# Performance work log

Measured on AMD Instinct MI355X. Metric: run time of the kernel, lower is better.

Reference implementation:

```python
import jax, jax.numpy as jnp
import numpy as np

B, N, H = 4, 512, 64
EDGE_IN = 2 * H + 4

def silu(x):
    return x * jax.nn.sigmoid(x)

def setup_inputs() -> dict:
    key = jax.random.key(0)
    ks = jax.random.split(key, 16)
    def w(k, fan_in, fan_out):
        return (jax.random.normal(k, (fan_in, fan_out), jnp.float32) / np.sqrt(fan_in)).astype(jnp.float32)
    return {
        "h":   jax.random.normal(ks[0], (B, N, H), jnp.float32),
        "pos": jax.random.normal(ks[1], (B, N, 2), jnp.float32),
        "vel": jax.random.normal(ks[2], (B, N, 2), jnp.float32),
        # edge_mlp: Linear(2H+4,H) SiLU Linear(H,H) SiLU
        "ew1": w(ks[3], EDGE_IN, H), "eb1": jnp.zeros((H,), jnp.float32),
        "ew2": w(ks[4], H, H),       "eb2": jnp.zeros((H,), jnp.float32),
        # force_mlp: Linear(H,H) SiLU Linear(H,1)
        "fw1": w(ks[5], H, H),       "fb1": jnp.zeros((H,), jnp.float32),
        "fw2": w(ks[6], H, 1),       "fb2": jnp.zeros((1,), jnp.float32),
        # node_mlp: Linear(2H,H) SiLU Linear(H,H)
        "nw1": w(ks[7], 2 * H, H),   "nb1": jnp.zeros((H,), jnp.float32),
        "nw2": w(ks[8], H, H),       "nb2": jnp.zeros((H,), jnp.float32),
    }

def reference(h, pos, vel, ew1, eb1, ew2, eb2, fw1, fb1, fw2, fb2, nw1, nb1, nw2, nb2):
    b, n, hd = h.shape
    # rel_pos[b,i,j] = pos[b,j] - pos[b,i]  (torch: pos.unsqueeze(1) - pos.unsqueeze(2))
    rel_pos = pos[:, None, :, :] - pos[:, :, None, :]                # (B,N,N,2)
    dist_sq = jnp.sum(rel_pos ** 2, axis=-1, keepdims=True)         # (B,N,N,1)
    dist = jnp.sqrt(dist_sq + 1e-8)
    normal = rel_pos / dist                                          # (B,N,N,2)
    speed_sq = jnp.sum(vel ** 2, axis=-1, keepdims=True)             # (B,N,1)
    rel_vel = vel[:, None, :, :] - vel[:, :, None, :]                # (B,N,N,2)
    approach = jnp.sum(rel_vel * normal, axis=-1, keepdims=True)     # (B,N,N,1)
    h_i = jnp.broadcast_to(h[:, :, None, :], (b, n, n, hd))
    h_j = jnp.broadcast_to(h[:, None, :, :], (b, n, n, hd))
    sp_i = jnp.broadcast_to(speed_sq[:, :, None, :], (b, n, n, 1))
    sp_j = jnp.broadcast_to(speed_sq[:, None, :, :], (b, n, n, 1))
    edge_feat = jnp.concatenate([h_i, h_j, dist_sq, sp_i, sp_j, approach], axis=-1)  # (B,N,N,2H+4)
    m_ij = silu(silu(edge_feat @ ew1 + eb1) @ ew2 + eb2)             # (B,N,N,H)
    force_weight = silu(m_ij @ fw1 + fb1) @ fw2 + fb2                # (B,N,N,1)
    force_ij = force_weight * normal                                 # (B,N,N,2)
    mask = (1.0 - jnp.eye(n, dtype=h.dtype))[None, :, :, None]       # zero self-edges
    force = jnp.sum(force_ij * mask, axis=2)                         # (B,N,2)
    m_agg = jnp.sum(m_ij * mask, axis=2)                             # (B,N,H)
    h_new = silu(jnp.concatenate([h, m_agg], axis=-1) @ nw1 + nb1) @ nw2 + nb2  # (B,N,H)
    return (h_new, force)
```

## Files before the change

### kernel.cpp

```cpp
#include <hip/hip_runtime.h>
#include <hip/hip_bf16.h>
#include <stdint.h>

#define NB 4
#define NN 512
#define NH 64

typedef __attribute__((ext_vector_type(4))) float f32x4;
typedef __attribute__((ext_vector_type(8))) short short8;

__device__ __forceinline__ unsigned short bf16b(float f){
  union { float f; uint32_t u; } c; c.f = f;
  uint32_t u = c.u;
  u += 0x7fffu + ((u >> 16) & 1u);
  return (unsigned short)(u >> 16);
}
__device__ __forceinline__ uint32_t pk2(float lo, float hi){
  return (uint32_t)bf16b(lo) | ((uint32_t)bf16b(hi) << 16);
}
__device__ __forceinline__ float silu(float x){
  float e = __expf(-x);
  return x * __builtin_amdgcn_rcpf(1.0f + e);
}

__global__ void k_precompute_ac(const float* __restrict__ h,
                                const float* __restrict__ vel,
                                const float* __restrict__ ew1,
                                const float* __restrict__ eb1,
                                float* __restrict__ wa, float* __restrict__ wc){
  const int row = blockIdx.x;
  const int t = threadIdx.x;
  const float* hr = h + row * NH;
  const float vx = vel[row*2], vy = vel[row*2+1];
  const float sp = vx*vx + vy*vy;
  float aa = eb1[t] + sp * ew1[129*NH + t];
  float cc =          sp * ew1[130*NH + t];
  #pragma unroll 8
  for (int k = 0; k < NH; ++k){
    float hk = hr[k];
    aa += hk * ew1[k*NH + t];
    cc += hk * ew1[(NH + k)*NH + t];
  }
  wa[row*NH + t] = aa;
  wc[row*NH + t] = cc;
}

__global__ void k_frag_weights(const float* __restrict__ ew2,
                               const float* __restrict__ fw1,
                               unsigned short* __restrict__ wef,
                               unsigned short* __restrict__ wff){
  const int idx = blockIdx.x * blockDim.x + threadIdx.x;
  const int mat = idx >> 12;
  const int r = idx & 4095;
  const int e2 = r & 7;
  const int lane = (r >> 3) & 63;
  const int mtkk = r >> 9;
  const int kk = mtkk >> 2, mt = mtkk & 3;
  const int krow = kk*32 + (lane >> 4)*8 + e2;
  const int col  = mt*16 + (lane & 15);
  const float* W = mat ? fw1 : ew2;
  unsigned short v = bf16b(W[krow*NH + col]);
  if (mat) wff[r] = v; else wef[r] = v;
}

__launch_bounds__(256)
__global__ void k_edges(const float* __restrict__ pos,
                        const float* __restrict__ vel,
                        const float* __restrict__ wa,
                        const float* __restrict__ wc,
                        const float* __restrict__ ew1,
                        const float* __restrict__ eb2,
                        const float* __restrict__ fb1,
                        const float* __restrict__ fw2,
                        const float* __restrict__ fb2,
                        const unsigned short* __restrict__ wef,
                        const unsigned short* __restrict__ wff,
                        float* __restrict__ wmagg,
                        float* __restrict__ outF){
  const int row = blockIdx.x;
  const int b = row >> 9;
  const int i = row & (NN - 1);
  const int tid = threadIdx.x;
  const int l = tid & 63;
  const int w = tid >> 6;
  const int e = l & 15;
  const int g = l >> 4;
  const int bN = b * NN;

  const float pix = pos[row*2], piy = pos[row*2+1];
  const float vix = vel[row*2], viy = vel[row*2+1];
  const float fb2s = fb2[0];

  const float* arow = wa + row * NH;
  const f32x4 af0a = *(const f32x4*)(arow + 8*g);
  const f32x4 af0b = *(const f32x4*)(arow + 8*g + 4);
  const f32x4 af1a = *(const f32x4*)(arow + 32 + 8*g);
  const f32x4 af1b = *(const f32x4*)(arow + 32 + 8*g + 4);
  const float* wD = ew1 + 128*NH;
  const f32x4 d0a = *(const f32x4*)(wD + 8*g);
  const f32x4 d0b = *(const f32x4*)(wD + 8*g + 4);
  const f32x4 d1a = *(const f32x4*)(wD + 32 + 8*g);
  const f32x4 d1b = *(const f32x4*)(wD + 32 + 8*g + 4);
  const float* wP = ew1 + 131*NH;
  const f32x4 p0a = *(const f32x4*)(wP + 8*g);
  const f32x4 p0b = *(const f32x4*)(wP + 8*g + 4);
  const f32x4 p1a = *(const f32x4*)(wP + 32 + 8*g);
  const f32x4 p1b = *(const f32x4*)(wP + 32 + 8*g + 4);

  short8 aw[2][4], fw[2][4];
  #pragma unroll
  for (int kk = 0; kk < 2; ++kk){
    #pragma unroll
    for (int mt = 0; mt < 4; ++mt){
      aw[kk][mt] = *(const short8*)(wef + ((kk*4 + mt)*64 + l)*8);
      fw[kk][mt] = *(const short8*)(wff + ((kk*4 + mt)*64 + l)*8);
    }
  }

  f32x4 magg[4];
  #pragma unroll
  for (int mt = 0; mt < 4; ++mt) magg[mt] = (f32x4){0.f,0.f,0.f,0.f};
  float fx = 0.f, fy = 0.f;

  for (int it = 0; it < 8; ++it){
    const int jbase = (w + 4*it) * 16;
    const int j = jbase + e;
    const float2 pj = *(const float2*)(pos + (bN + j)*2);
    const float2 vj = *(const float2*)(vel + (bN + j)*2);
    const float rx = pj.x - pix, ry = pj.y - piy;
    const float ds = rx*rx + ry*ry;
    const float inv = __builtin_amdgcn_rsqf(ds + 1e-8f);
    const float nx = rx*inv, ny = ry*inv;
    const float ap = (vj.x - vix)*nx + (vj.y - viy)*ny;
    const float maskv = (j != i) ? 1.0f : 0.0f;

    const float* crow = wc + (bN + j)*NH;
    const f32x4 c0a = *(const f32x4*)(crow + 8*g);
    const f32x4 c0b = *(const f32x4*)(crow + 8*g + 4);
    const f32x4 c1a = *(const f32x4*)(crow + 32 + 8*g);
    const f32x4 c1b = *(const f32x4*)(crow + 32 + 8*g + 4);

    short8 bx[2];
    {
      union { uint32_t u[4]; short8 s; } cv;
      float s0 = silu(af0a.x + c0a.x + ds*d0a.x + ap*p0a.x);
      float s1 = silu(af0a.y + c0a.y + ds*d0a.y + ap*p0a.y);
      float s2 = silu(af0a.z + c0a.z + ds*d0a.z + ap*p0a.z);
      float s3 = silu(af0a.w + c0a.w + ds*d0a.w + ap*p0a.w);
      cv.u[0] = pk2(s0, s1); cv.u[1] = pk2(s2, s3);
      float s4 = silu(af0b.x + c0b.x + ds*d0b.x + ap*p0b.x);
      float s5 = silu(af0b.y + c0b.y + ds*d0b.y + ap*p0b.y);
      float s6 = silu(af0b.z + c0b.z + ds*d0b.z + ap*p0b.z);
      float s7 = silu(af0b.w + c0b.w + ds*d0b.w + ap*p0b.w);
      cv.u[2] = pk2(s4, s5); cv.u[3] = pk2(s6, s7);
      bx[0] = cv.s;
    }
    {
      union { uint32_t u[4]; short8 s; } cv;
      float s0 = silu(af1a.x + c1a.x + ds*d1a.x + ap*p1a.x);
      float s1 = silu(af1a.y + c1a.y + ds*d1a.y + ap*p1a.y);
      float s2 = silu(af1a.z + c1a.z + ds*d1a.z + ap*p1a.z);
      float s3 = silu(af1a.w + c1a.w + ds*d1a.w + ap*p1a.w);
      cv.u[0] = pk2(s0, s1); cv.u[1] = pk2(s2, s3);
      float s4 = silu(af1b.x + c1b.x + ds*d1b.x + ap*p1b.x);
      float s5 = silu(af1b.y + c1b.y + ds*d1b.y + ap*p1b.y);
      float s6 = silu(af1b.z + c1b.z + ds*d1b.z + ap*p1b.z);
      float s7 = silu(af1b.w + c1b.w + ds*d1b.w + ap*p1b.w);
      cv.u[2] = pk2(s4, s5); cv.u[3] = pk2(s6, s7);
      bx[1] = cv.s;
    }

    f32x4 accm[4];
    #pragma unroll
    for (int mt = 0; mt < 4; ++mt){
      accm[mt] = *(const f32x4*)(eb2 + mt*16 + 4*g);
      accm[mt] = __builtin_amdgcn_mfma_f32_16x16x32_bf16(aw[0][mt], bx[0], accm[mt], 0, 0, 0);
      accm[mt] = __builtin_amdgcn_mfma_f32_16x16x32_bf16(aw[1][mt], bx[1], accm[mt], 0, 0, 0);
    }

    uint32_t pkm[4][2];
    #pragma unroll
    for (int mt = 0; mt < 4; ++mt){
      float m0 = silu(accm[mt].x);
      float m1 = silu(accm[mt].y);
      float m2 = silu(accm[mt].z);
      float m3 = silu(accm[mt].w);
      magg[mt].x += maskv * m0;
      magg[mt].y += maskv * m1;
      magg[mt].z += maskv * m2;
      magg[mt].w += maskv * m3;
      pkm[mt][0] = pk2(m0, m1);
      pkm[mt][1] = pk2(m2, m3);
    }

    short8 bm[2];
    #pragma unroll
    for (int kk = 0; kk < 2; ++kk){
      union { uint32_t u[4]; short8 s; } cv;
      #pragma unroll
      for (int s = 0; s < 4; ++s){
        const int srcLane = (((s >> 1) + 2*(g & 1)) << 4) + e;
        uint32_t v0 = (uint32_t)__shfl((int)pkm[2*kk    ][s & 1], srcLane);
        uint32_t v1 = (uint32_t)__shfl((int)pkm[2*kk + 1][s & 1], srcLane);
        cv.u[s] = (g < 2) ? v0 : v1;
      }
      bm[kk] = cv.s;
    }

    float p = 0.f;
    #pragma unroll
    for (int mt = 0; mt < 4; ++mt){
      f32x4 acc2 = *(const f32x4*)(fb1 + mt*16 + 4*g);
      acc2 = __builtin_amdgcn_mfma_f32_16x16x32_bf16(fw[0][mt], bm[0], acc2, 0, 0, 0);
      acc2 = __builtin_amdgcn_mfma_f32_16x16x32_bf16(fw[1][mt], bm[1], acc2, 0, 0, 0);
      const f32x4 f2v = *(const f32x4*)(fw2 + mt*16 + 4*g);
      p += silu(acc2.x) * f2v.x;
      p += silu(acc2.y) * f2v.y;
      p += silu(acc2.z) * f2v.z;
      p += silu(acc2.w) * f2v.w;
    }
    p += __shfl_xor(p, 16);
    p += __shfl_xor(p, 32);
    const float fwt = p + fb2s;
    fx += maskv * fwt * nx;
    fy += maskv * fwt * ny;
  }

  __shared__ float smagg[4][64];
  __shared__ float sforce[4][2];

  #pragma unroll
  for (int mt = 0; mt < 4; ++mt){
    #pragma unroll
    for (int r = 0; r < 4; ++r){
      float v = magg[mt][r];
      v += __shfl_xor(v, 1);
      v += __shfl_xor(v, 2);
      v += __shfl_xor(v, 4);
      v += __shfl_xor(v, 8);
      if (e == 0) smagg[w][mt*16 + 4*g + r] = v;
    }
  }
  fx += __shfl_xor(fx, 1); fx += __shfl_xor(fx, 2); fx += __shfl_xor(fx, 4); fx += __shfl_xor(fx, 8);
  fy += __shfl_xor(fy, 1); fy += __shfl_xor(fy, 2); fy += __shfl_xor(fy, 4); fy += __shfl_xor(fy, 8);
  if (l == 0){ sforce[w][0] = fx; sforce[w][1] = fy; }
  __syncthreads();

  if (tid < 64)
    wmagg[row*NH + tid] = smagg[0][tid] + smagg[1][tid] + smagg[2][tid] + smagg[3][tid];
  if (tid == 0){
    outF[row*2]     = sforce[0][0] + sforce[1][0] + sforce[2][0] + sforce[3][0];
    outF[row*2 + 1] = sforce[0][1] + sforce[1][1] + sforce[2][1] + sforce[3][1];
  }
}

__global__ void k_node(const float* __restrict__ h,
                       const float* __restrict__ wmagg,
                       const float* __restrict__ nw1,
                       const float* __restrict__ nb1,
                       const float* __restrict__ nw2,
                       const float* __restrict__ nb2,
                       float* __restrict__ outH){
  const int row = blockIdx.x;
  const int t = threadIdx.x;
  __shared__ float t1[64];
  const float* hr = h + row * NH;
  const float* mr = wmagg + row * NH;
  float acc = nb1[t];
  #pragma unroll 8
  for (int k = 0; k < NH; ++k) acc += hr[k] * nw1[k*NH + t];
  #pragma unroll 8
  for (int k = 0; k < NH; ++k) acc += mr[k] * nw1[(NH + k)*NH + t];
  t1[t] = silu(acc);
  __syncthreads();
  float o = nb2[t];
  #pragma unroll 8
  for (int k = 0; k < NH; ++k) o += t1[k] * nw2[k*NH + t];
  outH[row*NH + t] = o;
}

extern "C" void kernel_launch(void* const* d_in, const int* in_sizes, int n_in,
                              void* d_out, int out_size, void* d_ws, size_t ws_size,
                              hipStream_t stream){
  const float* h   = (const float*)d_in[0];
  const float* pos = (const float*)d_in[1];
  const float* vel = (const float*)d_in[2];
  const float* ew1 = (const float*)d_in[3];
  const float* eb1 = (const float*)d_in[4];
  const float* ew2 = (const float*)d_in[5];
  const float* eb2 = (const float*)d_in[6];
  const float* fw1 = (const float*)d_in[7];
  const float* fb1 = (const float*)d_in[8];
  const float* fw2 = (const float*)d_in[9];
  const float* fb2 = (const float*)d_in[10];
  const float* nw1 = (const float*)d_in[11];
  const float* nb1 = (const float*)d_in[12];
  const float* nw2 = (const float*)d_in[13];
  const float* nb2 = (const float*)d_in[14];
  float* out = (float*)d_out;

  float* wa    = (float*)d_ws;
  float* wc    = wa + NB*NN*NH;
  float* wmagg = wc + NB*NN*NH;
  unsigned short* wef = (unsigned short*)(wmagg + NB*NN*NH);
  unsigned short* wff = wef + 4096;

  k_precompute_ac<<<dim3(NB*NN), dim3(64), 0, stream>>>(h, vel, ew1, eb1, wa, wc);
  k_frag_weights<<<dim3(32), dim3(256), 0, stream>>>(ew2, fw1, wef, wff);
  k_edges<<<dim3(NB*NN), dim3(256), 0, stream>>>(pos, vel, wa, wc, ew1, eb2, fb1, fw2, fb2,
                                                 wef, wff, wmagg, out + NB*NN*NH);
  k_node<<<dim3(NB*NN), dim3(64), 0, stream>>>(h, wmagg, nw1, nb1, nw2, nb2, out);
}
```

Measured before the change: 188.5 us.

## Merge precompute kernels, prefetch edge loads, pack node rows, use bf16 intrinsic

Merges the two precompute kernels into one launch, with extra blocks converting the weight fragments. The edge loop now software-prefetches the next iteration's pos, vel and wc loads into registers and is kept rolled, and k_edges gets a min-blocks launch bound. The node kernel handles four rows per 256-thread block instead of one row per 64-thread block, and bf16 packing uses the HIP float2-to-bfloat162 intrinsic. These aim to cut launch overhead and hide load latency, at the cost of higher register pressure in the edge kernel.

```diff
diff --git a/kernel.cpp b/kernel.cpp
--- a/kernel.cpp
+++ b/kernel.cpp
@@ -16,20 +16,43 @@
   return (unsigned short)(u >> 16);
 }
 __device__ __forceinline__ uint32_t pk2(float lo, float hi){
-  return (uint32_t)bf16b(lo) | ((uint32_t)bf16b(hi) << 16);
+  __hip_bfloat162 h = __float22bfloat162_rn(make_float2(lo, hi));
+  union { __hip_bfloat162 h; uint32_t u; } c; c.h = h;
+  return c.u;
 }
 __device__ __forceinline__ float silu(float x){
   float e = __expf(-x);
   return x * __builtin_amdgcn_rcpf(1.0f + e);
 }
 
-__global__ void k_precompute_ac(const float* __restrict__ h,
-                                const float* __restrict__ vel,
-                                const float* __restrict__ ew1,
-                                const float* __restrict__ eb1,
-                                float* __restrict__ wa, float* __restrict__ wc){
-  const int row = blockIdx.x;
-  const int t = threadIdx.x;
+__launch_bounds__(256)
+__global__ void k_precompute(const float* __restrict__ h,
+                             const float* __restrict__ vel,
+                             const float* __restrict__ ew1,
+                             const float* __restrict__ eb1,
+                             const float* __restrict__ ew2,
+                             const float* __restrict__ fw1,
+                             float* __restrict__ wa, float* __restrict__ wc,
+                             unsigned short* __restrict__ wef,
+                             unsigned short* __restrict__ wff){
+  const int tid = threadIdx.x;
+  if (blockIdx.x >= 512){
+    const int idx = (blockIdx.x - 512) * 256 + tid;
+    const int mat = idx >> 12;
+    const int r = idx & 4095;
+    const int e2 = r & 7;
+    const int lane = (r >> 3) & 63;
+    const int mtkk = r >> 9;
+    const int kk = mtkk >> 2, mt = mtkk & 3;
+    const int krow = kk*32 + (lane >> 4)*8 + e2;
+    const int col  = mt*16 + (lane & 15);
+    const float* W = mat ? fw1 : ew2;
+    unsigned short v = bf16b(W[krow*NH + col]);
+    if (mat) wff[r] = v; else wef[r] = v;
+    return;
+  }
+  const int row = blockIdx.x * 4 + (tid >> 6);
+  const int t = tid & 63;
   const float* hr = h + row * NH;
   const float vx = vel[row*2], vy = vel[row*2+1];
   const float sp = vx*vx + vy*vy;
@@ -45,25 +68,7 @@
   wc[row*NH + t] = cc;
 }
 
-__global__ void k_frag_weights(const float* __restrict__ ew2,
-                               const float* __restrict__ fw1,
-                               unsigned short* __restrict__ wef,
-                               unsigned short* __restrict__ wff){
-  const int idx = blockIdx.x * blockDim.x + threadIdx.x;
-  const int mat = idx >> 12;
-  const int r = idx & 4095;
-  const int e2 = r & 7;
-  const int lane = (r >> 3) & 63;
-  const int mtkk = r >> 9;
-  const int kk = mtkk >> 2, mt = mtkk & 3;
-  const int krow = kk*32 + (lane >> 4)*8 + e2;
-  const int col  = mt*16 + (lane & 15);
-  const float* W = mat ? fw1 : ew2;
-  unsigned short v = bf16b(W[krow*NH + col]);
-  if (mat) wff[r] = v; else wef[r] = v;
-}
-
-__launch_bounds__(256)
+__launch_bounds__(256, 4)
 __global__ void k_edges(const float* __restrict__ pos,
                         const float* __restrict__ vel,
                         const float* __restrict__ wa,
@@ -122,23 +127,44 @@
   for (int mt = 0; mt < 4; ++mt) magg[mt] = (f32x4){0.f,0.f,0.f,0.f};
   float fx = 0.f, fy = 0.f;
 
+  float2 pj_n, vj_n;
+  f32x4 c0a_n, c0b_n, c1a_n, c1b_n;
+  {
+    const int j0 = w * 16 + e;
+    pj_n = *(const float2*)(pos + (bN + j0)*2);
+    vj_n = *(const float2*)(vel + (bN + j0)*2);
+    const float* crow = wc + (bN + j0)*NH;
+    c0a_n = *(const f32x4*)(crow + 8*g);
+    c0b_n = *(const f32x4*)(crow + 8*g + 4);
+    c1a_n = *(const f32x4*)(crow + 32 + 8*g);
+    c1b_n = *(const f32x4*)(crow + 32 + 8*g + 4);
+  }
+
+  #pragma unroll 1
   for (int it = 0; it < 8; ++it){
-    const int jbase = (w + 4*it) * 16;
-    const int j = jbase + e;
-    const float2 pj = *(const float2*)(pos + (bN + j)*2);
-    const float2 vj = *(const float2*)(vel + (bN + j)*2);
+    const int j = (w + 4*it) * 16 + e;
+    const float2 pj = pj_n;
+    const float2 vj = vj_n;
+    const f32x4 c0a = c0a_n, c0b = c0b_n, c1a = c1a_n, c1b = c1b_n;
+
+    {
+      const int itn = (it + 1) & 7;
+      const int jn = (w + 4*itn) * 16 + e;
+      pj_n = *(const float2*)(pos + (bN + jn)*2);
+      vj_n = *(const float2*)(vel + (bN + jn)*2);
+      const float* crn = wc + (bN + jn)*NH;
+      c0a_n = *(const f32x4*)(crn + 8*g);
+      c0b_n = *(const f32x4*)(crn + 8*g + 4);
+      c1a_n = *(const f32x4*)(crn + 32 + 8*g);
+      c1b_n = *(const f32x4*)(crn + 32 + 8*g + 4);
+    }
+
     const float rx = pj.x - pix, ry = pj.y - piy;
     const float ds = rx*rx + ry*ry;
     const float inv = __builtin_amdgcn_rsqf(ds + 1e-8f);
     const float nx = rx*inv, ny = ry*inv;
     const float ap = (vj.x - vix)*nx + (vj.y - viy)*ny;
     const float maskv = (j != i) ? 1.0f : 0.0f;
-
-    const float* crow = wc + (bN + j)*NH;
-    const f32x4 c0a = *(const f32x4*)(crow + 8*g);
-    const f32x4 c0b = *(const f32x4*)(crow + 8*g + 4);
-    const f32x4 c1a = *(const f32x4*)(crow + 32 + 8*g);
-    const f32x4 c1b = *(const f32x4*)(crow + 32 + 8*g + 4);
 
     short8 bx[2];
     {
@@ -254,6 +280,7 @@
   }
 }
 
+__launch_bounds__(256)
 __global__ void k_node(const float* __restrict__ h,
                        const float* __restrict__ wmagg,
                        const float* __restrict__ nw1,
@@ -261,9 +288,11 @@
                        const float* __restrict__ nw2,
                        const float* __restrict__ nb2,
                        float* __restrict__ outH){
-  const int row = blockIdx.x;
-  const int t = threadIdx.x;
-  __shared__ float t1[64];
+  const int tid = threadIdx.x;
+  const int r = tid >> 6;
+  const int row = blockIdx.x * 4 + r;
+  const int t = tid & 63;
+  __shared__ float t1[4][64];
   const float* hr = h + row * NH;
   const float* mr = wmagg + row * NH;
   float acc = nb1[t];
@@ -271,11 +300,11 @@
   for (int k = 0; k < NH; ++k) acc += hr[k] * nw1[k*NH + t];
   #pragma unroll 8
   for (int k = 0; k < NH; ++k) acc += mr[k] * nw1[(NH + k)*NH + t];
-  t1[t] = silu(acc);
+  t1[r][t] = silu(acc);
   __syncthreads();
   float o = nb2[t];
   #pragma unroll 8
-  for (int k = 0; k < NH; ++k) o += t1[k] * nw2[k*NH + t];
+  for (int k = 0; k < NH; ++k) o += t1[r][k] * nw2[k*NH + t];
   outH[row*NH + t] = o;
 }
 
@@ -305,9 +334,9 @@
   unsigned short* wef = (unsigned short*)(wmagg + NB*NN*NH);
   unsigned short* wff = wef + 4096;
 
-  k_precompute_ac<<<dim3(NB*NN), dim3(64), 0, stream>>>(h, vel, ew1, eb1, wa, wc);
-  k_frag_weights<<<dim3(32), dim3(256), 0, stream>>>(ew2, fw1, wef, wff);
+  k_precompute<<<dim3(544), dim3(256), 0, stream>>>(h, vel, ew1, eb1, ew2, fw1,
+                                                    wa, wc, wef, wff);
   k_edges<<<dim3(NB*NN), dim3(256), 0, stream>>>(pos, vel, wa, wc, ew1, eb2, fb1, fw2, fb2,
                                                  wef, wff, wmagg, out + NB*NN*NH);
-  k_node<<<dim3(NB*NN), dim3(64), 0, stream>>>(h, wmagg, nw1, nb1, nw2, nb2, out);
-}
+  k_node<<<dim3(512), dim3(256), 0, stream>>>(h, wmagg, nw1, nb1, nw2, nb2, out);
+}
```

Measured after the change: 355.2 us. 88.4% more time.
